# Optimization experiments

Hardware: AMD Instinct MI355X
Metric: run time of the kernel (lower is better)

Reference implementation:

```python
import jax, jax.numpy as jnp
import numpy as np
from jax.scipy.special import logsumexp

V, E, H, T, L = 50000, 256, 128, 64, 4096
D = int(np.log2(L))          # leaves live at heap level D
N = 2 * L - 1                # total nodes in perfect binary tree (heap indexing)


def _postorder(n_total):
    order = []
    def rec(i):
        if 2 * i + 1 < n_total:
            rec(2 * i + 1)
            rec(2 * i + 2)
        order.append(i)
    rec(0)
    return np.array(order, dtype=np.int32)

POST = _postorder(N)


def setup_inputs() -> dict:
    key = jax.random.key(0)
    ks = jax.random.split(key, 8)
    s = lambda k, shape, fan: (jax.random.normal(k, shape, jnp.float32) / np.sqrt(fan).astype(np.float32))
    return {
        "tokens": jax.random.randint(ks[0], (L,), 0, V),
        "emb": s(ks[1], (V, E), E),
        "W_ih": s(ks[2], (4 * H, E), E),
        "W_hh": s(ks[3], (4 * H, H), H),
        "b_ih": jnp.zeros((4 * H,), jnp.float32),
        "b_hh": jnp.zeros((4 * H,), jnp.float32),
        "W_p2h": s(ks[4], (H, 2 * H), 2 * H),
        "b_p2h": jnp.zeros((H,), jnp.float32),
        "W_uni": s(ks[5], (T, H), H),
        "b_uni": jnp.zeros((T,), jnp.float32),
        "W_edge": s(ks[6], (T * T, 2 * H), 2 * H),
        "b_edge": jnp.zeros((T * T,), jnp.float32),
    }


def reference(tokens, emb, W_ih, W_hh, b_ih, b_hh, W_p2h, b_p2h,
              W_uni, b_uni, W_edge, b_edge):
    # ---- Encoder: embedding + single-layer LSTM over the leaf sequence ----
    x = emb[tokens]                                   # [L, E]
    def step(carry, xt):
        h, c = carry
        g = W_ih @ xt + b_ih + W_hh @ h + b_hh        # torch gate order i,f,g,o
        i, f, gg, o = jnp.split(g, 4)
        c = jax.nn.sigmoid(f) * c + jax.nn.sigmoid(i) * jnp.tanh(gg)
        h = jax.nn.sigmoid(o) * jnp.tanh(c)
        return (h, c), h
    z = jnp.zeros((H,), x.dtype)
    _, leaf_h = jax.lax.scan(step, (z, z), x)         # [L, H]

    # ---- build_node_to_hidden: bottom-up per-level pair fusion ----
    hidden = jnp.zeros((N, H), x.dtype).at[L - 1:].set(leaf_h)
    for d in range(D - 1, -1, -1):
        idx = jnp.arange(2 ** d - 1, 2 ** (d + 1) - 1)
        pair = jnp.concatenate([hidden[2 * idx + 1], hidden[2 * idx + 2]], axis=1)
        hidden = hidden.at[idx].set(pair @ W_p2h.T + b_p2h)

    # ---- build_factors (batched over all nodes / edges) ----
    unary = hidden @ W_uni.T + b_uni                  # [N, T]
    child = jnp.arange(1, N)
    parent = (child - 1) // 2
    pair = jnp.concatenate([hidden[parent], hidden[child]], axis=1)
    edge_fac = (pair @ W_edge.T + b_edge).reshape(N - 1, T, T)  # edge (parent,child), idx = child-1

    # ---- upward pass (level-synchronous, bottom-up) ----
    v2f = unary                                       # node -> top factor message
    f2p = jnp.zeros((N, T), x.dtype)                  # factor -> parent message, indexed by child
    for d in range(D, -1, -1):
        idx = jnp.arange(2 ** d - 1, 2 ** (d + 1) - 1)
        if d < D:  # internal nodes: add both children's factor->node messages
            v2f = v2f.at[idx].add(f2p[2 * idx + 1] + f2p[2 * idx + 2])
        if d > 0:  # message through top edge factor to the parent
            f2p = f2p.at[idx].set(
                logsumexp(edge_fac[idx - 1] + v2f[idx][:, None, :], axis=2))

    # ---- downward pass (level-synchronous, top-down) ----
    f2n = jnp.zeros((N, T), x.dtype)                  # top-factor -> node message; root gets none
    for d in range(1, D + 1):
        idx = jnp.arange(2 ** d - 1, 2 ** (d + 1) - 1)
        par = (idx - 1) // 2
        sib = jnp.where(idx % 2 == 1, idx + 1, idx - 1)
        p2f = unary[par] + f2n[par] + f2p[sib]        # parent's messages, excluding this child's
        f2n = f2n.at[idx].set(
            logsumexp(edge_fac[idx - 1] + p2f[:, :, None], axis=1))

    beliefs = v2f + f2n                               # sum of all incoming messages, [N, T]
    return beliefs[POST]                              # stacked in postorder, like the original
```

## Files before the change

### kernel.cpp

```cpp
#include <hip/hip_runtime.h>
#include <hip/hip_bf16.h>

typedef __hip_bfloat16 bf16;
typedef float fx2 __attribute__((ext_vector_type(2)));

#define NL 4096
#define NH 128
#define NE 256
#define NT 64
#define NNODE 8191
#define NDEPTH 12

#define OF_WIH   0
#define OF_WHH   131072
#define OF_BIH   196608
#define OF_BHH   197120
#define OF_WP2H  197632
#define OF_BP2H  230400
#define OF_WUNI  230528
#define OF_BUNI  238720
#define OF_WEDGE 238784
#define OF_BEDGE 1287360
#define WF_TOTAL 1291456

__device__ __forceinline__ float b2f(bf16 x) { return __bfloat162float(x); }

__global__ void detect_kernel(const void* __restrict__ wedge_raw, int* __restrict__ flag) {
  __shared__ int cnt_sh[256];
  const unsigned short* p = (const unsigned short*)wedge_raw;
  int c = 0;
  for (int i = threadIdx.x; i < 32768; i += 256) {
    float v = __uint_as_float(((unsigned)p[2 * i]) << 16);
    if (fabsf(v) > 4.f) c++;
  }
  cnt_sh[threadIdx.x] = c;
  __syncthreads();
  for (int s = 128; s > 0; s >>= 1) {
    if (threadIdx.x < s) cnt_sh[threadIdx.x] += cnt_sh[threadIdx.x + s];
    __syncthreads();
  }
  if (threadIdx.x == 0) *flag = cnt_sh[0];
}

__global__ void convert_kernel(const void* s0, const void* s1, const void* s2, const void* s3,
                               const void* s4, const void* s5, const void* s6, const void* s7,
                               const void* s8, const void* s9,
                               const int* __restrict__ flag, float* __restrict__ wf) {
  int i = blockIdx.x * 256 + threadIdx.x;
  if (i >= WF_TOTAL) return;
  const void* src; int local;
  if      (i < OF_WHH)   { src = s0; local = i; }
  else if (i < OF_BIH)   { src = s1; local = i - OF_WHH; }
  else if (i < OF_BHH)   { src = s2; local = i - OF_BIH; }
  else if (i < OF_WP2H)  { src = s3; local = i - OF_BHH; }
  else if (i < OF_BP2H)  { src = s4; local = i - OF_WP2H; }
  else if (i < OF_WUNI)  { src = s5; local = i - OF_BP2H; }
  else if (i < OF_BUNI)  { src = s6; local = i - OF_WUNI; }
  else if (i < OF_WEDGE) { src = s7; local = i - OF_BUNI; }
  else if (i < OF_BEDGE) { src = s8; local = i - OF_WEDGE; }
  else                   { src = s9; local = i - OF_BEDGE; }
  bool isf32 = (*flag) > 100;
  wf[i] = isf32 ? ((const float*)src)[local] : b2f(((const bf16*)src)[local]);
}

__global__ __launch_bounds__(512) void g1_kernel(const int* __restrict__ tokens,
                                                 const void* __restrict__ emb_raw,
                                                 const int* __restrict__ flag,
                                                 const float* __restrict__ wf,
                                                 float* __restrict__ G1) {
  __shared__ __attribute__((aligned(16))) float xs[8 * NE];
  const bool isf32 = (*flag) > 100;
  const int t0 = blockIdx.x * 8;
  for (int q = threadIdx.x; q < 8 * NE; q += 512) {
    int tok = q >> 8, e = q & 255;
    size_t off = (size_t)tokens[t0 + tok] * NE + e;
    xs[q] = isf32 ? ((const float*)emb_raw)[off] : b2f(((const bf16*)emb_raw)[off]);
  }
  __syncthreads();
  const int r = threadIdx.x;
  const float bias = wf[OF_BIH + r] + wf[OF_BHH + r];
  float acc[8];
#pragma unroll
  for (int k = 0; k < 8; ++k) acc[k] = bias;
  const float4* W4 = (const float4*)(wf + OF_WIH + (size_t)r * NE);
#pragma unroll 8
  for (int j = 0; j < 64; ++j) {
    float4 wv = W4[j];
#pragma unroll
    for (int tok = 0; tok < 8; ++tok) {
      float4 xv = ((const float4*)(xs + tok * NE))[j];
      acc[tok] += wv.x * xv.x + wv.y * xv.y + wv.z * xv.z + wv.w * xv.w;
    }
  }
#pragma unroll
  for (int tok = 0; tok < 8; ++tok) G1[(size_t)(t0 + tok) * 512 + r] = acc[tok];
}

__global__ __launch_bounds__(512) void lstm_kernel(const float* __restrict__ wf,
                                                   const float* __restrict__ G1,
                                                   float* __restrict__ hidden) {
  const int r = threadIdx.x;
  __shared__ __attribute__((aligned(16))) float h_sh[NH];
  __shared__ float g_sh[512];
  fx2 w[64];
  const float4* W4 = (const float4*)(wf + OF_WHH + (size_t)r * NH);
#pragma unroll
  for (int j = 0; j < 32; ++j) {
    float4 v = W4[j];
    fx2 p0, p1; p0.x = v.x; p0.y = v.y; p1.x = v.z; p1.y = v.w;
    w[2 * j] = p0; w[2 * j + 1] = p1;
  }
  float c = 0.f;
  if (r < NH) h_sh[r] = 0.f;
  __syncthreads();
  float gnext = G1[r];
  for (int t = 0; t < NL; ++t) {
    float gcur = gnext;
    if (t + 1 < NL) gnext = G1[(size_t)(t + 1) * 512 + r];
    fx2 a0 = {0.f, 0.f}, a1 = {0.f, 0.f}, a2 = {0.f, 0.f}, a3 = {0.f, 0.f};
    const float4* h4 = (const float4*)h_sh;
#pragma unroll
    for (int j = 0; j < 16; ++j) {
      float4 h0 = h4[2 * j], h1 = h4[2 * j + 1];
      fx2 e0, e1, e2, e3;
      e0.x = h0.x; e0.y = h0.y; e1.x = h0.z; e1.y = h0.w;
      e2.x = h1.x; e2.y = h1.y; e3.x = h1.z; e3.y = h1.w;
      a0 += w[4 * j + 0] * e0;
      a1 += w[4 * j + 1] * e1;
      a2 += w[4 * j + 2] * e2;
      a3 += w[4 * j + 3] * e3;
    }
    g_sh[r] = gcur + (a0.x + a0.y) + (a1.x + a1.y) + (a2.x + a2.y) + (a3.x + a3.y);
    __syncthreads();
    if (r < NH) {
      float iv = g_sh[r], fv = g_sh[r + 128], gv = g_sh[r + 256], ov = g_sh[r + 384];
      float si = 1.f / (1.f + __expf(-iv));
      float sf = 1.f / (1.f + __expf(-fv));
      float tg = 1.f - 2.f / (__expf(2.f * gv) + 1.f);
      float so = 1.f / (1.f + __expf(-ov));
      c = sf * c + si * tg;
      float hh = so * (1.f - 2.f / (__expf(2.f * c) + 1.f));
      h_sh[r] = hh;
      hidden[(size_t)(NL - 1 + t) * NH + r] = hh;
    }
    __syncthreads();
  }
}

__global__ void p2h_kernel(const float* __restrict__ wf, float* __restrict__ hidden, int base) {
  int node = base + blockIdx.x;
  int j = threadIdx.x;
  __shared__ __attribute__((aligned(16))) float pr[2 * NH];
  const float* hl = hidden + (size_t)(2 * node + 1) * NH;
  pr[j] = hl[j];
  pr[j + NH] = hl[j + NH];
  __syncthreads();
  float acc = wf[OF_BP2H + j];
  const float4* W4 = (const float4*)(wf + OF_WP2H + (size_t)j * 2 * NH);
  const float4* p4 = (const float4*)pr;
#pragma unroll 16
  for (int q = 0; q < 64; ++q) {
    float4 u = W4[q], x = p4[q];
    acc += u.x * x.x + u.y * x.y + u.z * x.z + u.w * x.w;
  }
  hidden[(size_t)node * NH + j] = acc;
}

__global__ void unary_kernel(const float* __restrict__ wf, const float* __restrict__ hidden,
                             float* __restrict__ unary, float* __restrict__ f2n) {
  int node = blockIdx.x;
  int ct = threadIdx.x;
  __shared__ __attribute__((aligned(16))) float hs[NH];
  hs[ct] = hidden[(size_t)node * NH + ct];
  hs[ct + 64] = hidden[(size_t)node * NH + 64 + ct];
  __syncthreads();
  float acc = wf[OF_BUNI + ct];
  const float4* W4 = (const float4*)(wf + OF_WUNI + (size_t)ct * NH);
  const float4* h4 = (const float4*)hs;
#pragma unroll
  for (int q = 0; q < 32; ++q) {
    float4 u = W4[q], x = h4[q];
    acc += u.x * x.x + u.y * x.y + u.z * x.z + u.w * x.w;
  }
  unary[(size_t)node * NT + ct] = acc;
  if (node == 0) f2n[ct] = 0.f;
}

__global__ __launch_bounds__(256) void edge_kernel(const float* __restrict__ hidden,
                                                   const float* __restrict__ wf,
                                                   float* __restrict__ edge) {
  __shared__ __attribute__((aligned(16))) float As[32][132];
  __shared__ __attribute__((aligned(16))) float Bs[32][132];
  const int tid = threadIdx.x;
  const int nb = blockIdx.x;
  const int mb = blockIdx.y;
  const int tm = tid >> 4, tn = tid & 15;
  float acc[8][8];
#pragma unroll
  for (int i = 0; i < 8; ++i)
#pragma unroll
    for (int j = 0; j < 8; ++j) acc[i][j] = 0.f;
  const int sr = tid >> 1;
  const int sq = tid & 1;
  for (int ch = 0; ch < 8; ++ch) {
    {
      int gm = mb * 128 + sr;
      const float* srcA = (ch < 4) ? hidden + (size_t)(gm >> 1) * NH + ch * 32
                                   : hidden + (size_t)(gm + 1) * NH + (ch - 4) * 32;
      bool ok = (gm < NNODE - 1);
#pragma unroll
      for (int i = 0; i < 4; ++i) {
        int kk = sq * 16 + i * 4;
        float4 v = ok ? *(const float4*)(srcA + kk) : make_float4(0.f, 0.f, 0.f, 0.f);
        As[kk + 0][sr] = v.x; As[kk + 1][sr] = v.y; As[kk + 2][sr] = v.z; As[kk + 3][sr] = v.w;
      }
    }
    {
      int gn = nb * 128 + sr;
      const float* srcB = wf + OF_WEDGE + (size_t)gn * NE + ch * 32;
#pragma unroll
      for (int i = 0; i < 4; ++i) {
        int kk = sq * 16 + i * 4;
        float4 v = *(const float4*)(srcB + kk);
        Bs[kk + 0][sr] = v.x; Bs[kk + 1][sr] = v.y; Bs[kk + 2][sr] = v.z; Bs[kk + 3][sr] = v.w;
      }
    }
    __syncthreads();
#pragma unroll 8
    for (int kk = 0; kk < 32; ++kk) {
      float a[8], b[8];
      *(float4*)(a)     = *(const float4*)&As[kk][tm * 4];
      *(float4*)(a + 4) = *(const float4*)&As[kk][64 + tm * 4];
      *(float4*)(b)     = *(const float4*)&Bs[kk][tn * 4];
      *(float4*)(b + 4) = *(const float4*)&Bs[kk][64 + tn * 4];
#pragma unroll
      for (int i = 0; i < 8; ++i)
#pragma unroll
        for (int j = 0; j < 8; ++j) acc[i][j] += a[i] * b[j];
    }
    __syncthreads();
  }
  float bias[8];
#pragma unroll
  for (int j = 0; j < 8; ++j)
    bias[j] = wf[OF_BEDGE + nb * 128 + (j >> 2) * 64 + tn * 4 + (j & 3)];
#pragma unroll
  for (int i = 0; i < 8; ++i) {
    int gm = mb * 128 + (i >> 2) * 64 + tm * 4 + (i & 3);
    if (gm < NNODE - 1) {
      float* row = edge + (size_t)gm * 4096 + nb * 128;
      float4 o0, o1;
      o0.x = acc[i][0] + bias[0]; o0.y = acc[i][1] + bias[1];
      o0.z = acc[i][2] + bias[2]; o0.w = acc[i][3] + bias[3];
      o1.x = acc[i][4] + bias[4]; o1.y = acc[i][5] + bias[5];
      o1.z = acc[i][6] + bias[6]; o1.w = acc[i][7] + bias[7];
      *(float4*)(row + tn * 4) = o0;
      *(float4*)(row + 64 + tn * 4) = o1;
    }
  }
}

__global__ void up_kernel(const float* __restrict__ unary, const float* __restrict__ edge,
                          float* __restrict__ v2f, float* __restrict__ f2p,
                          int base, int depth) {
  int node = base + blockIdx.x;
  int tid = threadIdx.x;
  __shared__ __attribute__((aligned(16))) float vs[NT];
  float vv = unary[(size_t)node * NT + tid];
  if (depth < NDEPTH)
    vv += f2p[(size_t)(2 * node + 1) * NT + tid] + f2p[(size_t)(2 * node + 2) * NT + tid];
  v2f[(size_t)node * NT + tid] = vv;
  vs[tid] = vv;
  __syncthreads();
  if (depth == 0) return;
  const float4* E4 = (const float4*)(edge + (size_t)(node - 1) * 4096 + tid * 64);
  const float4* v4 = (const float4*)vs;
  float x[NT];
#pragma unroll
  for (int q = 0; q < 16; ++q) {
    float4 e = E4[q], vq = v4[q];
    x[4 * q + 0] = e.x + vq.x; x[4 * q + 1] = e.y + vq.y;
    x[4 * q + 2] = e.z + vq.z; x[4 * q + 3] = e.w + vq.w;
  }
  float m = x[0];
#pragma unroll
  for (int i = 1; i < NT; ++i) m = fmaxf(m, x[i]);
  float s = 0.f;
#pragma unroll
  for (int i = 0; i < NT; ++i) s += __expf(x[i] - m);
  f2p[(size_t)node * NT + tid] = m + __logf(s);
}

__global__ void down_kernel(const float* __restrict__ unary, const float* __restrict__ edge,
                            const float* __restrict__ f2p, float* __restrict__ f2n,
                            int base) {
  int node = base + blockIdx.x;
  int tid = threadIdx.x;
  int par = (node - 1) >> 1;
  int sib = (node & 1) ? node + 1 : node - 1;
  __shared__ __attribute__((aligned(16))) float us[NT];
  us[tid] = unary[(size_t)par * NT + tid] + f2n[(size_t)par * NT + tid] +
            f2p[(size_t)sib * NT + tid];
  __syncthreads();
  float uu[NT];
  const float4* u4 = (const float4*)us;
#pragma unroll
  for (int q = 0; q < 16; ++q) {
    float4 t4 = u4[q];
    uu[4 * q] = t4.x; uu[4 * q + 1] = t4.y; uu[4 * q + 2] = t4.z; uu[4 * q + 3] = t4.w;
  }
  const float* E = edge + (size_t)(node - 1) * 4096 + tid;
  float x[NT];
#pragma unroll
  for (int p = 0; p < NT; ++p) x[p] = E[(size_t)p * 64] + uu[p];
  float m = x[0];
#pragma unroll
  for (int i = 1; i < NT; ++i) m = fmaxf(m, x[i]);
  float s = 0.f;
#pragma unroll
  for (int i = 0; i < NT; ++i) s += __expf(x[i] - m);
  f2n[(size_t)node * NT + tid] = m + __logf(s);
}

__global__ void final_kernel(const float* __restrict__ v2f, const float* __restrict__ f2n,
                             const int* __restrict__ flag, void* __restrict__ out) {
  int node = blockIdx.x;
  int tid = threadIdx.x;
  unsigned v = (unsigned)node + 1u;
  int d = 31 - __clz((int)v);
  int b0 = 0, S = NNODE;
  for (int b = d - 1; b >= 0; --b) {
    int sz = (S - 1) >> 1;
    if ((v >> b) & 1) b0 += sz;
    S = sz;
  }
  int pos = b0 + S - 1;
  float val = v2f[(size_t)node * NT + tid] + f2n[(size_t)node * NT + tid];
  if ((*flag) > 100) ((float*)out)[(size_t)pos * NT + tid] = val;
  else               ((bf16*)out)[(size_t)pos * NT + tid] = __float2bfloat16(val);
}

extern "C" void kernel_launch(void* const* d_in, const int* in_sizes, int n_in,
                              void* d_out, int out_size, void* d_ws, size_t ws_size,
                              hipStream_t stream) {
  (void)in_sizes; (void)n_in; (void)out_size; (void)ws_size;
  const int* tokens = (const int*)d_in[0];

  float* ws     = (float*)d_ws;
  int*   flag   = (int*)ws;
  float* wf     = ws + 16;
  float* hidden = wf + WF_TOTAL;
  float* G1     = hidden + (size_t)NNODE * NH;
  float* unary  = G1 + (size_t)NL * 512;
  float* v2f    = unary + (size_t)NNODE * NT;
  float* f2p    = v2f + (size_t)NNODE * NT;
  float* f2n    = f2p + (size_t)NNODE * NT;
  float* edge   = f2n + (size_t)NNODE * NT;

  detect_kernel<<<1, 256, 0, stream>>>(d_in[10], flag);
  convert_kernel<<<(WF_TOTAL + 255) / 256, 256, 0, stream>>>(
      d_in[2], d_in[3], d_in[4], d_in[5], d_in[6], d_in[7],
      d_in[8], d_in[9], d_in[10], d_in[11], flag, wf);
  g1_kernel<<<NL / 8, 512, 0, stream>>>(tokens, d_in[1], flag, wf, G1);
  lstm_kernel<<<1, 512, 0, stream>>>(wf, G1, hidden);
  for (int d = NDEPTH - 1; d >= 0; --d)
    p2h_kernel<<<1 << d, 128, 0, stream>>>(wf, hidden, (1 << d) - 1);
  unary_kernel<<<NNODE, 64, 0, stream>>>(wf, hidden, unary, f2n);
  edge_kernel<<<dim3(32, 64), 256, 0, stream>>>(hidden, wf, edge);
  for (int d = NDEPTH; d >= 0; --d)
    up_kernel<<<1 << d, 64, 0, stream>>>(unary, edge, v2f, f2p, (1 << d) - 1, d);
  for (int d = 1; d <= NDEPTH; ++d)
    down_kernel<<<1 << d, 64, 0, stream>>>(unary, edge, f2p, f2n, (1 << d) - 1);
  final_kernel<<<NNODE, 64, 0, stream>>>(v2f, f2n, flag, d_out);
}
```

Before: 4.081 ms.

## Split LSTM recurrent matvec across 1024 threads with partial-sum reduction

The sequential LSTM kernel now runs with 1024 threads, where each gate row's dot product over the hidden state is split into two halves. Partial sums are combined through shared memory before the gate nonlinearities. Each thread keeps half as many weights in explicitly pinned registers, which is meant to shorten the per-step dot-product latency on the serial critical path. The cost is a larger block, more shared-memory traffic for the partials, and barrier synchronisation across twice as many waves.

```diff
diff --git a/kernel.cpp b/kernel.cpp
--- a/kernel.cpp
+++ b/kernel.cpp
@@ -96,55 +96,74 @@
   for (int tok = 0; tok < 8; ++tok) G1[(size_t)(t0 + tok) * 512 + r] = acc[tok];
 }
 
-__global__ __launch_bounds__(512) void lstm_kernel(const float* __restrict__ wf,
-                                                   const float* __restrict__ G1,
-                                                   float* __restrict__ hidden) {
-  const int r = threadIdx.x;
+__global__ __launch_bounds__(1024, 4) void lstm_kernel(const float* __restrict__ wf,
+                                                       const float* __restrict__ G1,
+                                                       float* __restrict__ hidden) {
+  const int tid  = threadIdx.x;
+  const int r    = tid & 511;
+  const int half = tid >> 9;
   __shared__ __attribute__((aligned(16))) float h_sh[NH];
-  __shared__ float g_sh[512];
-  fx2 w[64];
-  const float4* W4 = (const float4*)(wf + OF_WHH + (size_t)r * NH);
-#pragma unroll
-  for (int j = 0; j < 32; ++j) {
-    float4 v = W4[j];
-    fx2 p0, p1; p0.x = v.x; p0.y = v.y; p1.x = v.z; p1.y = v.w;
-    w[2 * j] = p0; w[2 * j + 1] = p1;
-  }
+  __shared__ __attribute__((aligned(16))) float part_sh[1024];
+
+  const float4* W4 = (const float4*)(wf + OF_WHH + (size_t)r * NH + half * 64);
+  fx2 w00, w01, w02, w03, w04, w05, w06, w07, w08, w09, w10, w11, w12, w13, w14, w15,
+      w16, w17, w18, w19, w20, w21, w22, w23, w24, w25, w26, w27, w28, w29, w30, w31;
+#define LDW(i, wa, wb) { float4 v = W4[i]; wa.x = v.x; wa.y = v.y; wb.x = v.z; wb.y = v.w; }
+  LDW(0,  w00, w01) LDW(1,  w02, w03) LDW(2,  w04, w05) LDW(3,  w06, w07)
+  LDW(4,  w08, w09) LDW(5,  w10, w11) LDW(6,  w12, w13) LDW(7,  w14, w15)
+  LDW(8,  w16, w17) LDW(9,  w18, w19) LDW(10, w20, w21) LDW(11, w22, w23)
+  LDW(12, w24, w25) LDW(13, w26, w27) LDW(14, w28, w29) LDW(15, w30, w31)
+#undef LDW
+#define PIN(x) asm volatile("" : "+v"(x));
+  PIN(w00) PIN(w01) PIN(w02) PIN(w03) PIN(w04) PIN(w05) PIN(w06) PIN(w07)
+  PIN(w08) PIN(w09) PIN(w10) PIN(w11) PIN(w12) PIN(w13) PIN(w14) PIN(w15)
+  PIN(w16) PIN(w17) PIN(w18) PIN(w19) PIN(w20) PIN(w21) PIN(w22) PIN(w23)
+  PIN(w24) PIN(w25) PIN(w26) PIN(w27) PIN(w28) PIN(w29) PIN(w30) PIN(w31)
+#undef PIN
+
   float c = 0.f;
-  if (r < NH) h_sh[r] = 0.f;
-  __syncthreads();
-  float gnext = G1[r];
+  if (tid < NH) h_sh[tid] = 0.f;
+  __syncthreads();
+  float gnext = (half == 0) ? G1[r] : 0.f;
+#define FMA4(j, wa, wb, wc, wd) {                                        \
+    float4 h0 = h4[2 * (j)], h1 = h4[2 * (j) + 1];                       \
+    fx2 e0, e1, e2, e3;                                                  \
+    e0.x = h0.x; e0.y = h0.y; e1.x = h0.z; e1.y = h0.w;                  \
+    e2.x = h1.x; e2.y = h1.y; e3.x = h1.z; e3.y = h1.w;                  \
+    a0 += (wa) * e0; a1 += (wb) * e1; a2 += (wc) * e2; a3 += (wd) * e3; }
   for (int t = 0; t < NL; ++t) {
     float gcur = gnext;
-    if (t + 1 < NL) gnext = G1[(size_t)(t + 1) * 512 + r];
+    if (half == 0 && t + 1 < NL) gnext = G1[(size_t)(t + 1) * 512 + r];
     fx2 a0 = {0.f, 0.f}, a1 = {0.f, 0.f}, a2 = {0.f, 0.f}, a3 = {0.f, 0.f};
-    const float4* h4 = (const float4*)h_sh;
-#pragma unroll
-    for (int j = 0; j < 16; ++j) {
-      float4 h0 = h4[2 * j], h1 = h4[2 * j + 1];
-      fx2 e0, e1, e2, e3;
-      e0.x = h0.x; e0.y = h0.y; e1.x = h0.z; e1.y = h0.w;
-      e2.x = h1.x; e2.y = h1.y; e3.x = h1.z; e3.y = h1.w;
-      a0 += w[4 * j + 0] * e0;
-      a1 += w[4 * j + 1] * e1;
-      a2 += w[4 * j + 2] * e2;
-      a3 += w[4 * j + 3] * e3;
-    }
-    g_sh[r] = gcur + (a0.x + a0.y) + (a1.x + a1.y) + (a2.x + a2.y) + (a3.x + a3.y);
-    __syncthreads();
-    if (r < NH) {
-      float iv = g_sh[r], fv = g_sh[r + 128], gv = g_sh[r + 256], ov = g_sh[r + 384];
+    const float4* h4 = (const float4*)(h_sh + (half << 6));
+    FMA4(0, w00, w01, w02, w03)
+    FMA4(1, w04, w05, w06, w07)
+    FMA4(2, w08, w09, w10, w11)
+    FMA4(3, w12, w13, w14, w15)
+    FMA4(4, w16, w17, w18, w19)
+    FMA4(5, w20, w21, w22, w23)
+    FMA4(6, w24, w25, w26, w27)
+    FMA4(7, w28, w29, w30, w31)
+    float part = (a0.x + a0.y) + (a1.x + a1.y) + (a2.x + a2.y) + (a3.x + a3.y);
+    part_sh[tid] = half ? part : part + gcur;
+    __syncthreads();
+    if (tid < NH) {
+      float iv = part_sh[tid]       + part_sh[tid + 512];
+      float fv = part_sh[tid + 128] + part_sh[tid + 640];
+      float gv = part_sh[tid + 256] + part_sh[tid + 768];
+      float ov = part_sh[tid + 384] + part_sh[tid + 896];
       float si = 1.f / (1.f + __expf(-iv));
       float sf = 1.f / (1.f + __expf(-fv));
       float tg = 1.f - 2.f / (__expf(2.f * gv) + 1.f);
       float so = 1.f / (1.f + __expf(-ov));
       c = sf * c + si * tg;
       float hh = so * (1.f - 2.f / (__expf(2.f * c) + 1.f));
-      h_sh[r] = hh;
-      hidden[(size_t)(NL - 1 + t) * NH + r] = hh;
-    }
-    __syncthreads();
-  }
+      h_sh[tid] = hh;
+      hidden[(size_t)(NL - 1 + t) * NH + tid] = hh;
+    }
+    __syncthreads();
+  }
+#undef FMA4
 }
 
 __global__ void p2h_kernel(const float* __restrict__ wf, float* __restrict__ hidden, int base) {
@@ -362,7 +381,7 @@
       d_in[2], d_in[3], d_in[4], d_in[5], d_in[6], d_in[7],
       d_in[8], d_in[9], d_in[10], d_in[11], flag, wf);
   g1_kernel<<<NL / 8, 512, 0, stream>>>(tokens, d_in[1], flag, wf, G1);
-  lstm_kernel<<<1, 512, 0, stream>>>(wf, G1, hidden);
+  lstm_kernel<<<1, 1024, 0, stream>>>(wf, G1, hidden);
   for (int d = NDEPTH - 1; d >= 0; --d)
     p2h_kernel<<<1 << d, 128, 0, stream>>>(wf, hidden, (1 << d) - 1);
   unary_kernel<<<NNODE, 64, 0, stream>>>(wf, hidden, unary, f2n);
```

Measured after the change: 4.281 ms. 1.05x slower.

## Regroup LSTM recurrence so each hidden unit's four gates reduce together

Applied to the files above, without the earlier changes.

G1 is now written gate-interleaved per hidden unit, and the LSTM kernel assigns four threads per hidden unit. Each thread computes partial dot products for all four gates over a 32-element slice of h, then combines them with wave shuffles, so a single float4 holds the gates. The recurrent weights are no longer held in registers. They are streamed each step from global memory, as raw bf16 or as converted fp32 depending on the detected input type. This is meant to cut register pressure and shared-memory traffic. In exchange, every timestep now reloads the weights from cache.

```diff
diff --git a/kernel.cpp b/kernel.cpp
--- a/kernel.cpp
+++ b/kernel.cpp
@@ -24,6 +24,8 @@
 #define WF_TOTAL 1291456
 
 __device__ __forceinline__ float b2f(bf16 x) { return __bfloat162float(x); }
+__device__ __forceinline__ float blo(unsigned u) { return __uint_as_float(u << 16); }
+__device__ __forceinline__ float bhi(unsigned u) { return __uint_as_float(u & 0xffff0000u); }
 
 __global__ void detect_kernel(const void* __restrict__ wedge_raw, int* __restrict__ flag) {
   __shared__ int cnt_sh[256];
@@ -92,58 +94,140 @@
       acc[tok] += wv.x * xv.x + wv.y * xv.y + wv.z * xv.z + wv.w * xv.w;
     }
   }
-#pragma unroll
-  for (int tok = 0; tok < 8; ++tok) G1[(size_t)(t0 + tok) * 512 + r] = acc[tok];
+  const int gi = (r & 127) * 4 + (r >> 7);
+#pragma unroll
+  for (int tok = 0; tok < 8; ++tok) G1[(size_t)(t0 + tok) * 512 + gi] = acc[tok];
 }
 
 __global__ __launch_bounds__(512) void lstm_kernel(const float* __restrict__ wf,
+                                                   const void* __restrict__ whh_raw,
+                                                   const int* __restrict__ flag,
                                                    const float* __restrict__ G1,
                                                    float* __restrict__ hidden) {
-  const int r = threadIdx.x;
+  const int r  = threadIdx.x;
+  const int j  = r >> 2;
+  const int kq = r & 3;
+  __shared__ __attribute__((aligned(16))) float4 g_sh[NH];
   __shared__ __attribute__((aligned(16))) float h_sh[NH];
-  __shared__ float g_sh[512];
-  fx2 w[64];
-  const float4* W4 = (const float4*)(wf + OF_WHH + (size_t)r * NH);
-#pragma unroll
-  for (int j = 0; j < 32; ++j) {
-    float4 v = W4[j];
-    fx2 p0, p1; p0.x = v.x; p0.y = v.y; p1.x = v.z; p1.y = v.w;
-    w[2 * j] = p0; w[2 * j + 1] = p1;
-  }
+  const bool isf32 = (*flag) > 100;
+
   float c = 0.f;
   if (r < NH) h_sh[r] = 0.f;
   __syncthreads();
-  float gnext = G1[r];
-  for (int t = 0; t < NL; ++t) {
-    float gcur = gnext;
-    if (t + 1 < NL) gnext = G1[(size_t)(t + 1) * 512 + r];
-    fx2 a0 = {0.f, 0.f}, a1 = {0.f, 0.f}, a2 = {0.f, 0.f}, a3 = {0.f, 0.f};
-    const float4* h4 = (const float4*)h_sh;
-#pragma unroll
-    for (int j = 0; j < 16; ++j) {
-      float4 h0 = h4[2 * j], h1 = h4[2 * j + 1];
-      fx2 e0, e1, e2, e3;
-      e0.x = h0.x; e0.y = h0.y; e1.x = h0.z; e1.y = h0.w;
-      e2.x = h1.x; e2.y = h1.y; e3.x = h1.z; e3.y = h1.w;
-      a0 += w[4 * j + 0] * e0;
-      a1 += w[4 * j + 1] * e1;
-      a2 += w[4 * j + 2] * e2;
-      a3 += w[4 * j + 3] * e3;
-    }
-    g_sh[r] = gcur + (a0.x + a0.y) + (a1.x + a1.y) + (a2.x + a2.y) + (a3.x + a3.y);
-    __syncthreads();
-    if (r < NH) {
-      float iv = g_sh[r], fv = g_sh[r + 128], gv = g_sh[r + 256], ov = g_sh[r + 384];
-      float si = 1.f / (1.f + __expf(-iv));
-      float sf = 1.f / (1.f + __expf(-fv));
-      float tg = 1.f - 2.f / (__expf(2.f * gv) + 1.f);
-      float so = 1.f / (1.f + __expf(-ov));
-      c = sf * c + si * tg;
-      float hh = so * (1.f - 2.f / (__expf(2.f * c) + 1.f));
-      h_sh[r] = hh;
-      hidden[(size_t)(NL - 1 + t) * NH + r] = hh;
-    }
-    __syncthreads();
+
+  if (!isf32) {
+    const unsigned short* wb = (const unsigned short*)whh_raw;
+    const uint4* Wp0 = (const uint4*)(wb + (size_t)(0 * 128 + j) * NH + kq * 32);
+    const uint4* Wp1 = (const uint4*)(wb + (size_t)(1 * 128 + j) * NH + kq * 32);
+    const uint4* Wp2 = (const uint4*)(wb + (size_t)(2 * 128 + j) * NH + kq * 32);
+    const uint4* Wp3 = (const uint4*)(wb + (size_t)(3 * 128 + j) * NH + kq * 32);
+    float4 gnext = make_float4(0.f, 0.f, 0.f, 0.f);
+    if (kq == 0) gnext = *(const float4*)(G1 + 4 * j);
+    for (int t = 0; t < NL; ++t) {
+      float4 gcur = gnext;
+      if (kq == 0 && t + 1 < NL)
+        gnext = *(const float4*)(G1 + (size_t)(t + 1) * 512 + 4 * j);
+      const float4* h4 = (const float4*)(h_sh + kq * 32);
+      float4 hv0 = h4[0], hv1 = h4[1], hv2 = h4[2], hv3 = h4[3];
+      float4 hv4 = h4[4], hv5 = h4[5], hv6 = h4[6], hv7 = h4[7];
+      fx2 a0 = {0.f, 0.f}, a1 = {0.f, 0.f}, a2 = {0.f, 0.f}, a3 = {0.f, 0.f};
+#define QMAC(i, hA, hB) {                                                   \
+      fx2 e01, e23, e45, e67;                                               \
+      e01.x = hA.x; e01.y = hA.y; e23.x = hA.z; e23.y = hA.w;               \
+      e45.x = hB.x; e45.y = hB.y; e67.x = hB.z; e67.y = hB.w;               \
+      { uint4 wq = Wp0[i]; fx2 w01, w23, w45, w67;                          \
+        w01.x = blo(wq.x); w01.y = bhi(wq.x); w23.x = blo(wq.y); w23.y = bhi(wq.y); \
+        w45.x = blo(wq.z); w45.y = bhi(wq.z); w67.x = blo(wq.w); w67.y = bhi(wq.w); \
+        a0 += w01 * e01; a0 += w23 * e23; a0 += w45 * e45; a0 += w67 * e67; } \
+      { uint4 wq = Wp1[i]; fx2 w01, w23, w45, w67;                          \
+        w01.x = blo(wq.x); w01.y = bhi(wq.x); w23.x = blo(wq.y); w23.y = bhi(wq.y); \
+        w45.x = blo(wq.z); w45.y = bhi(wq.z); w67.x = blo(wq.w); w67.y = bhi(wq.w); \
+        a1 += w01 * e01; a1 += w23 * e23; a1 += w45 * e45; a1 += w67 * e67; } \
+      { uint4 wq = Wp2[i]; fx2 w01, w23, w45, w67;                          \
+        w01.x = blo(wq.x); w01.y = bhi(wq.x); w23.x = blo(wq.y); w23.y = bhi(wq.y); \
+        w45.x = blo(wq.z); w45.y = bhi(wq.z); w67.x = blo(wq.w); w67.y = bhi(wq.w); \
+        a2 += w01 * e01; a2 += w23 * e23; a2 += w45 * e45; a2 += w67 * e67; } \
+      { uint4 wq = Wp3[i]; fx2 w01, w23, w45, w67;                          \
+        w01.x = blo(wq.x); w01.y = bhi(wq.x); w23.x = blo(wq.y); w23.y = bhi(wq.y); \
+        w45.x = blo(wq.z); w45.y = bhi(wq.z); w67.x = blo(wq.w); w67.y = bhi(wq.w); \
+        a3 += w01 * e01; a3 += w23 * e23; a3 += w45 * e45; a3 += w67 * e67; } }
+      QMAC(0, hv0, hv1)
+      QMAC(1, hv2, hv3)
+      QMAC(2, hv4, hv5)
+      QMAC(3, hv6, hv7)
+#undef QMAC
+      float s0 = a0.x + a0.y, s1 = a1.x + a1.y, s2 = a2.x + a2.y, s3 = a3.x + a3.y;
+      s0 += __shfl_xor(s0, 1); s1 += __shfl_xor(s1, 1);
+      s2 += __shfl_xor(s2, 1); s3 += __shfl_xor(s3, 1);
+      s0 += __shfl_xor(s0, 2); s1 += __shfl_xor(s1, 2);
+      s2 += __shfl_xor(s2, 2); s3 += __shfl_xor(s3, 2);
+      if (kq == 0) {
+        float4 gf;
+        gf.x = s0 + gcur.x; gf.y = s1 + gcur.y;
+        gf.z = s2 + gcur.z; gf.w = s3 + gcur.w;
+        g_sh[j] = gf;
+      }
+      __syncthreads();
+      if (r < NH) {
+        float4 g = g_sh[r];
+        float si = 1.f / (1.f + __expf(-g.x));
+        float sf = 1.f / (1.f + __expf(-g.y));
+        float tg = 1.f - 2.f / (__expf(2.f * g.z) + 1.f);
+        float so = 1.f / (1.f + __expf(-g.w));
+        c = sf * c + si * tg;
+        float hh = so * (1.f - 2.f / (__expf(2.f * c) + 1.f));
+        h_sh[r] = hh;
+        hidden[(size_t)(NL - 1 + t) * NH + r] = hh;
+      }
+      __syncthreads();
+    }
+  } else {
+    const float* base = wf + OF_WHH;
+    const float4* Fp0 = (const float4*)(base + (size_t)(0 * 128 + j) * NH + kq * 32);
+    const float4* Fp1 = (const float4*)(base + (size_t)(1 * 128 + j) * NH + kq * 32);
+    const float4* Fp2 = (const float4*)(base + (size_t)(2 * 128 + j) * NH + kq * 32);
+    const float4* Fp3 = (const float4*)(base + (size_t)(3 * 128 + j) * NH + kq * 32);
+    float4 gnext = make_float4(0.f, 0.f, 0.f, 0.f);
+    if (kq == 0) gnext = *(const float4*)(G1 + 4 * j);
+    for (int t = 0; t < NL; ++t) {
+      float4 gcur = gnext;
+      if (kq == 0 && t + 1 < NL)
+        gnext = *(const float4*)(G1 + (size_t)(t + 1) * 512 + 4 * j);
+      const float4* h4 = (const float4*)(h_sh + kq * 32);
+      float s0 = 0.f, s1 = 0.f, s2 = 0.f, s3 = 0.f;
+#pragma unroll
+      for (int i = 0; i < 8; ++i) {
+        float4 hq = h4[i];
+        float4 w0 = Fp0[i], w1 = Fp1[i], w2 = Fp2[i], w3 = Fp3[i];
+        s0 += w0.x * hq.x + w0.y * hq.y + w0.z * hq.z + w0.w * hq.w;
+        s1 += w1.x * hq.x + w1.y * hq.y + w1.z * hq.z + w1.w * hq.w;
+        s2 += w2.x * hq.x + w2.y * hq.y + w2.z * hq.z + w2.w * hq.w;
+        s3 += w3.x * hq.x + w3.y * hq.y + w3.z * hq.z + w3.w * hq.w;
+      }
+      s0 += __shfl_xor(s0, 1); s1 += __shfl_xor(s1, 1);
+      s2 += __shfl_xor(s2, 1); s3 += __shfl_xor(s3, 1);
+      s0 += __shfl_xor(s0, 2); s1 += __shfl_xor(s1, 2);
+      s2 += __shfl_xor(s2, 2); s3 += __shfl_xor(s3, 2);
+      if (kq == 0) {
+        float4 gf;
+        gf.x = s0 + gcur.x; gf.y = s1 + gcur.y;
+        gf.z = s2 + gcur.z; gf.w = s3 + gcur.w;
+        g_sh[j] = gf;
+      }
+      __syncthreads();
+      if (r < NH) {
+        float4 g = g_sh[r];
+        float si = 1.f / (1.f + __expf(-g.x));
+        float sf = 1.f / (1.f + __expf(-g.y));
+        float tg = 1.f - 2.f / (__expf(2.f * g.z) + 1.f);
+        float so = 1.f / (1.f + __expf(-g.w));
+        c = sf * c + si * tg;
+        float hh = so * (1.f - 2.f / (__expf(2.f * c) + 1.f));
+        h_sh[r] = hh;
+        hidden[(size_t)(NL - 1 + t) * NH + r] = hh;
+      }
+      __syncthreads();
+    }
   }
 }
 
@@ -362,7 +446,7 @@
       d_in[2], d_in[3], d_in[4], d_in[5], d_in[6], d_in[7],
       d_in[8], d_in[9], d_in[10], d_in[11], flag, wf);
   g1_kernel<<<NL / 8, 512, 0, stream>>>(tokens, d_in[1], flag, wf, G1);
-  lstm_kernel<<<1, 512, 0, stream>>>(wf, G1, hidden);
+  lstm_kernel<<<1, 512, 0, stream>>>(wf, d_in[3], flag, G1, hidden);
   for (int d = NDEPTH - 1; d >= 0; --d)
     p2h_kernel<<<1 << d, 128, 0, stream>>>(wf, hidden, (1 << d) - 1);
   unary_kernel<<<NNODE, 64, 0, stream>>>(wf, hidden, unary, f2n);
```

New measurement: 4.019 ms. No clear change (-1.5%).
